# Kernel tuning notes

Hardware: AMD Instinct MI355X
Metric: run time of the kernel (lower is better)

## Reference

```python
import jax, jax.numpy as jnp
import numpy as np

B, N, F, H, ITERS = 128, 512, 8, 128, 3


def setup_inputs() -> dict:
    key = jax.random.key(0)
    ks = jax.random.split(key, 20)
    s = lambda d: 1.0 / np.sqrt(d)
    inp = {
        "jets": jax.random.normal(ks[0], (B, N, F), dtype=jnp.float32),
        "mask": jnp.ones((B, N), dtype=jnp.float32),
        # embedding: 2-layer MLP (emb_init=2)
        "emb_W0": jax.random.normal(ks[1], (F, H), jnp.float32) * s(F),
        "emb_b0": jnp.zeros((H,), jnp.float32),
        "emb_W1": jax.random.normal(ks[2], (H, H), jnp.float32) * s(H),
        "emb_b1": jnp.zeros((H,), jnp.float32),
        # MP layers (stacked over iters): message MLP + vertex update MLP
        "mp_Wm": jax.random.normal(ks[3], (ITERS, H, H), jnp.float32) * s(H),
        "mp_bm": jnp.zeros((ITERS, H), jnp.float32),
        "mp_Wu": jax.random.normal(ks[4], (ITERS, 2 * H, H), jnp.float32) * s(2 * H),
        "mp_bu": jnp.zeros((ITERS, H), jnp.float32),
        # simple readout: sum-pool then 2-layer MLP
        "ro_W1": jax.random.normal(ks[5], (H, H), jnp.float32) * s(H),
        "ro_b1": jnp.zeros((H,), jnp.float32),
        "ro_W2": jax.random.normal(ks[6], (H, H), jnp.float32) * s(H),
        "ro_b2": jnp.zeros((H,), jnp.float32),
    }
    return inp


def _adjacency(jets, mask):
    # fixed Gaussian-kernel affinity on raw features, row-softmax normalized
    sq = jnp.sum(jets * jets, axis=-1)                      # [B,N]
    d2 = sq[:, :, None] + sq[:, None, :] - 2.0 * jnp.einsum("bif,bjf->bij", jets, jets)
    logits = -d2 + jnp.where(mask[:, None, :] > 0, 0.0, -1e9)  # mask columns
    return jax.nn.softmax(logits, axis=-1)                  # [B,N,N]


def reference(jets, mask, emb_W0, emb_b0, emb_W1, emb_b1,
              mp_Wm, mp_bm, mp_Wu, mp_bu, ro_W1, ro_b1, ro_W2, ro_b2):
    # embedding
    h = jax.nn.relu(jnp.einsum("bnf,fh->bnh", jets, emb_W0) + emb_b0)
    h = jax.nn.relu(jnp.einsum("bnh,hk->bnk", h, emb_W1) + emb_b1)
    dij = _adjacency(jets, mask)                            # fixed across iterations
    m3 = mask[:, :, None]
    for t in range(ITERS):  # small fixed iteration count
        msg = jax.nn.relu(jnp.einsum("bnh,hk->bnk", h, mp_Wm[t]) + mp_bm[t])
        agg = jnp.einsum("bij,bjh->bih", dij, msg)          # gather+aggregate over adjacency
        h = jax.nn.relu(jnp.einsum("bnh,hk->bnk", jnp.concatenate([h, agg], axis=-1), mp_Wu[t]) + mp_bu[t])
        h = h * m3
    pooled = jnp.sum(h * m3, axis=1)                        # [B,H]
    out = jax.nn.relu(pooled @ ro_W1 + ro_b1) @ ro_W2 + ro_b2
    return out
```

## Files before the change

kernel.cpp:

```cpp
#include <hip/hip_runtime.h>
#include <stdint.h>
#include <stddef.h>

#define Bb 128
#define Nn 512
#define Hh 128
#define ROWS (Bb*Nn)

typedef __bf16 bf16;
typedef __bf16 bf16x2 __attribute__((ext_vector_type(2)));
typedef __bf16 bf16x4 __attribute__((ext_vector_type(4)));
typedef __bf16 bf16x8 __attribute__((ext_vector_type(8)));
typedef float  f32x4  __attribute__((ext_vector_type(4)));

__device__ __forceinline__ void glds16(const void* g, void* l) {
  __builtin_amdgcn_global_load_lds(
      (const __attribute__((address_space(1))) void*)g,
      (__attribute__((address_space(3))) void*)l, 16, 0, 0);
}


__global__ __launch_bounds__(256) void prep_pmat(
    const float* __restrict__ eW1, const float* __restrict__ Wm,
    const float* __restrict__ Wu, bf16* __restrict__ WTe,
    bf16* __restrict__ WmF, bf16* __restrict__ WuF,
    const float* __restrict__ jets, const float* __restrict__ mask,
    bf16* __restrict__ PF, float* __restrict__ rsum) {
  __shared__ float Xs[Nn*9];
  __shared__ float cbs[Nn];
  const int t = threadIdx.x;
  if (blockIdx.x >= 512) {
    int idx = (blockIdx.x - 512)*256 + t;
    if (idx < 16384) {
      int k = idx >> 7, c = idx & 127;
      WTe[c*128 + (k ^ ((c & 7) << 3))] = (bf16)eW1[idx];
    } else if (idx < 65536) {
      int sub = idx - 16384;
      int s = sub >> 14, r = sub & 16383;
      int k = r >> 7, c = r & 127;
      WmF[s*16384 + (((c>>4)*4 + (k>>5))*64 + ((k>>3)&3)*16 + (c&15))*8 + (k&7)] = (bf16)Wm[sub];
    } else {
      int sub = idx - 65536;
      int s = sub >> 15, r = sub & 32767;
      int k = r >> 7, c = r & 127;
      WuF[s*32768 + (((c>>4)*8 + (k>>5))*64 + ((k>>3)&3)*16 + (c&15))*8 + (k&7)] = (bf16)Wu[sub];
    }
    return;
  }
  const int b = blockIdx.x & 127, ic = blockIdx.x >> 7;
  const int i0 = ic*128;
  const float* jb = jets + (size_t)b*Nn*8;
  for (int j = t; j < Nn; j += 256) {
    float s2 = 0.f;
#pragma unroll
    for (int f = 0; f < 8; ++f) { float v = jb[j*8+f]; Xs[j*9+f] = v; s2 = fmaf(v,v,s2); }
    cbs[j] = s2 + (mask[(size_t)b*Nn+j] > 0.f ? 0.f : 1e9f);
  }
  __syncthreads();
  const int w = t >> 6, lane = t & 63, l15 = lane & 15, g = lane >> 4;
  const int i0w = i0 + w*32;
  float xi2[2][8], sqi[2], lsum[2];
#pragma unroll
  for (int r = 0; r < 2; ++r) {
    int i = i0w + r*16 + l15;
    float sq = 0.f;
#pragma unroll
    for (int f = 0; f < 8; ++f) {
      float v = Xs[i*9+f];
      xi2[r][f] = 2.f*v;
      sq = fmaf(v, v, sq);
    }
    sqi[r] = sq;
    lsum[r] = 0.f;
  }
  bf16* Pr[2];
#pragma unroll
  for (int r = 0; r < 2; ++r) {
    int it = (i0w >> 4) + r;
    Pr[r] = PF + (((size_t)b*32 + it)*16)*512 + lane*8;
  }
#pragma unroll 2
  for (int j0 = 0; j0 < Nn; j0 += 32) {
    bf16x8 pfr[2];
#pragma unroll
    for (int e = 0; e < 8; ++e) {
      int j = j0 + 8*g + e;
      float xj[8];
#pragma unroll
      for (int f = 0; f < 8; ++f) xj[f] = Xs[j*9+f];
      float cb = cbs[j];
      float d0 = -(cb + sqi[0]);
      float d1 = -(cb + sqi[1]);
#pragma unroll
      for (int f = 0; f < 8; ++f) {
        d0 = fmaf(xi2[0][f], xj[f], d0);
        d1 = fmaf(xi2[1][f], xj[f], d1);
      }
      float ev0 = __expf(d0), ev1 = __expf(d1);
      lsum[0] += ev0; lsum[1] += ev1;
      pfr[0][e] = (bf16)ev0;
      pfr[1][e] = (bf16)ev1;
    }
#pragma unroll
    for (int r = 0; r < 2; ++r)
      *(bf16x8*)(Pr[r] + (j0 >> 5)*512) = pfr[r];
  }
#pragma unroll
  for (int r = 0; r < 2; ++r) {
    float s = lsum[r];
    s += __shfl_xor(s, 16, 64);
    s += __shfl_xor(s, 32, 64);
    if (g == 0) rsum[(size_t)b*Nn + i0w + r*16 + l15] = 1.f/s;
  }
}

__global__ __launch_bounds__(256) void embed_msg0(
    const float* __restrict__ jets, const float* __restrict__ W0,
    const float* __restrict__ b0, const bf16* __restrict__ WTe,
    const float* __restrict__ b1, const bf16* __restrict__ WmF0,
    const float* __restrict__ bm0, bf16* __restrict__ h,
    bf16* __restrict__ msgF) {
  __shared__ float sW0[8*128];
  __shared__ float sb0[128];
  __shared__ bf16 h0s[128*128];
  __shared__ bf16 sWT[128*128];
  const int t = threadIdx.x;
  const int w = t >> 6, lane = t & 63, l15 = lane & 15, g = lane >> 4;
  const int row_blk = blockIdx.x*128;
  for (int q = w; q < 32; q += 4)
    glds16((const char*)WTe + q*1024 + lane*16, (char*)(void*)sWT + q*1024);
  for (int i = t; i < 8*128; i += 256) sW0[i] = W0[i];
  if (t < 128) sb0[t] = b0[t];
  __syncthreads();
  {
    const int row = t & 127, colbase = (t >> 7) * 64;
    const float4* jp = (const float4*)(jets + ((size_t)row_blk + row)*8);
    float4 x0 = jp[0], x1 = jp[1];
    float x[8] = {x0.x,x0.y,x0.z,x0.w,x1.x,x1.y,x1.z,x1.w};
    const int sw = (row & 7) << 3;
#pragma unroll
    for (int cg = 0; cg < 16; ++cg) {
      int c0 = colbase + cg*4;
      bf16x4 o;
#pragma unroll
      for (int j = 0; j < 4; ++j) {
        float a = sb0[c0+j];
#pragma unroll
        for (int f = 0; f < 8; ++f) a = fmaf(x[f], sW0[f*128 + c0 + j], a);
        o[j] = (bf16)fmaxf(a, 0.f);
      }
      *(bf16x4*)(h0s + row*128 + (c0 ^ sw)) = o;
    }
  }
  __syncthreads();
  const int wr = (w & 1)*64, wc = (w >> 1)*64;
  f32x4 acc[4][4];
#pragma unroll
  for (int m = 0; m < 4; ++m)
#pragma unroll
    for (int n = 0; n < 4; ++n) acc[m][n] = (f32x4){0.f,0.f,0.f,0.f};
#pragma unroll
  for (int kk = 0; kk < 128; kk += 32) {
    bf16x8 bfr[4], wfr[4];
#pragma unroll
    for (int n = 0; n < 4; ++n) {
      int row = wr + n*16 + l15;
      bfr[n] = *(const bf16x8*)(h0s + row*128 + ((kk + 8*g) ^ ((row & 7) << 3)));
    }
#pragma unroll
    for (int m = 0; m < 4; ++m) {
      int c = wc + m*16 + l15;
      wfr[m] = *(const bf16x8*)(sWT + c*128 + ((kk + 8*g) ^ ((c & 7) << 3)));
    }
#pragma unroll
    for (int m = 0; m < 4; ++m)
#pragma unroll
      for (int n = 0; n < 4; ++n)
        acc[m][n] = __builtin_amdgcn_mfma_f32_16x16x32_bf16(wfr[m], bfr[n], acc[m][n], 0,0,0);
  }
  __syncthreads();
#pragma unroll
  for (int m = 0; m < 4; ++m) {
    f32x4 bs = *(const f32x4*)(b1 + wc + m*16 + g*4);
#pragma unroll
    for (int n = 0; n < 4; ++n) {
      int lr = wr + n*16 + l15;
      int r = row_blk + lr;
      int c0 = wc + m*16 + g*4;
      bf16x4 o;
#pragma unroll
      for (int j = 0; j < 4; ++j) o[j] = (bf16)fmaxf(acc[m][n][j] + bs[j], 0.f);
      *(bf16x4*)(h + (size_t)r*128 + c0) = o;
      *(bf16x4*)(h0s + lr*128 + (c0 ^ ((lr & 7) << 3))) = o;
    }
  }
  __syncthreads();
  {
    f32x4 acc2[4][4];
#pragma unroll
    for (int m = 0; m < 4; ++m)
#pragma unroll
      for (int n = 0; n < 4; ++n) acc2[m][n] = (f32x4){0.f,0.f,0.f,0.f};
#pragma unroll
    for (int kk = 0; kk < 128; kk += 32) {
      bf16x8 bfr[4], wfr[4];
#pragma unroll
      for (int n = 0; n < 4; ++n) {
        int lr = wr + n*16 + l15;
        bfr[n] = *(const bf16x8*)(h0s + lr*128 + ((kk + 8*g) ^ ((lr & 7) << 3)));
      }
#pragma unroll
      for (int m = 0; m < 4; ++m) {
        int cblk = (wc >> 4) + m;
        wfr[m] = *(const bf16x8*)(WmF0 + (size_t)(cblk*4 + (kk >> 5))*512 + lane*8);
      }
#pragma unroll
      for (int m = 0; m < 4; ++m)
#pragma unroll
        for (int n = 0; n < 4; ++n)
          acc2[m][n] = __builtin_amdgcn_mfma_f32_16x16x32_bf16(bfr[n], wfr[m], acc2[m][n], 0,0,0);
    }
    const int b = row_blk >> 9;
    const int rbase = (row_blk & 511) + wr;
#pragma unroll
    for (int m = 0; m < 4; ++m) {
      int c = wc + m*16 + l15;
      int mblk = (wc >> 4) + m;
      float bc = bm0[c];
#pragma unroll
      for (int n = 0; n < 4; ++n) {
        int rl = rbase + n*16 + g*4;
        bf16x4 o;
#pragma unroll
        for (int j = 0; j < 4; ++j) o[j] = (bf16)fmaxf(acc2[m][n][j] + bc, 0.f);
        size_t off = (size_t)b*65536 + (size_t)((rl>>5)*8 + mblk)*512
                   + (((rl>>3)&3)*16 + l15)*8 + (rl&7);
        *(bf16x4*)(msgF + off) = o;
      }
    }
  }
}

template<bool DO_MSG>
__global__ __launch_bounds__(256, 1) void iter_fused(
    const bf16* __restrict__ PF, const float* __restrict__ rsum,
    const float* __restrict__ mask, const bf16* __restrict__ msgFin,
    bf16* __restrict__ h,
    const bf16* __restrict__ WuF, const float* __restrict__ bu,
    const bf16* __restrict__ WmF, const float* __restrict__ bm,
    bf16* __restrict__ msgFout) {
  __shared__ __align__(16) char smem[65536];
  bf16* htile = (bf16*)smem;
  bf16* aggs  = (bf16*)(smem + 32768);
  const int t = threadIdx.x;
  const int b  = blockIdx.x & 127;
  const int ic = blockIdx.x >> 7;
  const int i0 = ic*128;
  const int w = t >> 6, lane = t & 63, l15 = lane & 15, g = lane >> 4;

  {
    const int i0w = i0 + w*32;
    float r_i[2];
#pragma unroll
    for (int r = 0; r < 2; ++r) r_i[r] = rsum[(size_t)b*Nn + i0w + r*16 + l15];
    f32x4 acc[2][8];
#pragma unroll
    for (int r = 0; r < 2; ++r)
#pragma unroll
      for (int m = 0; m < 8; ++m) acc[r][m] = (f32x4){0.f,0.f,0.f,0.f};
    const bf16* mBF = msgFin + (size_t)b*65536 + lane*8;
    const bf16* pBF = PF + ((size_t)b*32 + (i0w >> 4))*16*512 + lane*8;

    bf16x8 afrA[8], afrB[8], pfrA[2], pfrB[2];
    auto loadA = [&](int kt) {
#pragma unroll
      for (int m = 0; m < 8; ++m) afrA[m] = *(const bf16x8*)(mBF + (kt*8 + m)*512);
      pfrA[0] = *(const bf16x8*)(pBF + kt*512);
      pfrA[1] = *(const bf16x8*)(pBF + (16 + kt)*512);
    };
    auto loadB = [&](int kt) {
#pragma unroll
      for (int m = 0; m < 8; ++m) afrB[m] = *(const bf16x8*)(mBF + (kt*8 + m)*512);
      pfrB[0] = *(const bf16x8*)(pBF + kt*512);
      pfrB[1] = *(const bf16x8*)(pBF + (16 + kt)*512);
    };
    auto compute = [&](const bf16x8* afr, const bf16x8* pfr) {
#pragma unroll
      for (int m = 0; m < 8; ++m) {
        acc[0][m] = __builtin_amdgcn_mfma_f32_16x16x32_bf16(afr[m], pfr[0], acc[0][m], 0,0,0);
        acc[1][m] = __builtin_amdgcn_mfma_f32_16x16x32_bf16(afr[m], pfr[1], acc[1][m], 0,0,0);
      }
    };

    loadA(0);
#pragma unroll
    for (int kt = 0; kt < 16; kt += 2) {
      loadB(kt + 1);
      compute(afrA, pfrA);
      if (kt + 2 < 16) loadA(kt + 2);
      compute(afrB, pfrB);
    }
#pragma unroll
    for (int r = 0; r < 2; ++r) {
      int lr = w*32 + r*16 + l15;
#pragma unroll
      for (int m = 0; m < 8; ++m) {
        bf16x4 o;
#pragma unroll
        for (int j = 0; j < 4; ++j) o[j] = (bf16)(acc[r][m][j] * r_i[r]);
        int c0 = m*16 + g*4;
        *(bf16x4*)(aggs + lr*128 + (c0 ^ ((lr & 7) << 3))) = o;
      }
    }
  }
  __syncthreads();

  const int wr = (w & 1)*64, wc = (w >> 1)*64;
  const size_t growbase = (size_t)b*Nn + i0;
  {
    f32x4 acc[4][4];
#pragma unroll
    for (int m = 0; m < 4; ++m)
#pragma unroll
      for (int n = 0; n < 4; ++n) acc[m][n] = (f32x4){0.f,0.f,0.f,0.f};
#pragma unroll
    for (int kk = 0; kk < 256; kk += 32) {
      bf16x8 bfr[4];
      if (kk < 128) {
#pragma unroll
        for (int n = 0; n < 4; ++n)
          bfr[n] = *(const bf16x8*)(h + (growbase + wr + n*16 + l15)*128 + kk + 8*g);
      } else {
#pragma unroll
        for (int n = 0; n < 4; ++n) {
          int lr = wr + n*16 + l15;
          int kl = (kk - 128) + 8*g;
          bfr[n] = *(const bf16x8*)(aggs + lr*128 + (kl ^ ((lr & 7) << 3)));
        }
      }
      bf16x8 wfr[4];
#pragma unroll
      for (int m = 0; m < 4; ++m) {
        int cblk = (wc >> 4) + m;
        wfr[m] = *(const bf16x8*)(WuF + (size_t)(cblk*8 + (kk >> 5))*512 + lane*8);
      }
#pragma unroll
      for (int m = 0; m < 4; ++m)
#pragma unroll
        for (int n = 0; n < 4; ++n)
          acc[m][n] = __builtin_amdgcn_mfma_f32_16x16x32_bf16(wfr[m], bfr[n], acc[m][n], 0,0,0);
    }
    __syncthreads();
#pragma unroll
    for (int m = 0; m < 4; ++m) {
      f32x4 bs = *(const f32x4*)(bu + wc + m*16 + g*4);
#pragma unroll
      for (int n = 0; n < 4; ++n) {
        int lr = wr + n*16 + l15;
        size_t r = growbase + lr;
        float mv = mask[r];
        bf16x4 o;
#pragma unroll
        for (int j = 0; j < 4; ++j)
          o[j] = (bf16)(fmaxf(acc[m][n][j] + bs[j], 0.f) * mv);
        int c0 = wc + m*16 + g*4;
        *(bf16x4*)(h + r*128 + c0) = o;
        if (DO_MSG)
          *(bf16x4*)(htile + lr*128 + (c0 ^ ((lr & 7) << 3))) = o;
      }
    }
  }
  if (!DO_MSG) return;
  __syncthreads();

  {
    f32x4 acc[4][4];
#pragma unroll
    for (int m = 0; m < 4; ++m)
#pragma unroll
      for (int n = 0; n < 4; ++n) acc[m][n] = (f32x4){0.f,0.f,0.f,0.f};
#pragma unroll
    for (int kk = 0; kk < 128; kk += 32) {
      bf16x8 bfr[4], wfr[4];
#pragma unroll
      for (int n = 0; n < 4; ++n) {
        int lr = wr + n*16 + l15;
        bfr[n] = *(const bf16x8*)(htile + lr*128 + ((kk + 8*g) ^ ((lr & 7) << 3)));
      }
#pragma unroll
      for (int m = 0; m < 4; ++m) {
        int cblk = (wc >> 4) + m;
        wfr[m] = *(const bf16x8*)(WmF + (size_t)(cblk*4 + (kk >> 5))*512 + lane*8);
      }
#pragma unroll
      for (int m = 0; m < 4; ++m)
#pragma unroll
        for (int n = 0; n < 4; ++n)
          acc[m][n] = __builtin_amdgcn_mfma_f32_16x16x32_bf16(bfr[n], wfr[m], acc[m][n], 0,0,0);
    }
#pragma unroll
    for (int m = 0; m < 4; ++m) {
      int c = wc + m*16 + l15;
      int mblk = (wc >> 4) + m;
      float bc = bm[c];
#pragma unroll
      for (int n = 0; n < 4; ++n) {
        int rl = i0 + wr + n*16 + g*4;
        bf16x4 o;
#pragma unroll
        for (int j = 0; j < 4; ++j) o[j] = (bf16)fmaxf(acc[m][n][j] + bc, 0.f);
        size_t off = (size_t)b*65536 + (size_t)((rl>>5)*8 + mblk)*512
                   + (((rl>>3)&3)*16 + l15)*8 + (rl&7);
        *(bf16x4*)(msgFout + off) = o;
      }
    }
  }
}

__global__ __launch_bounds__(256) void pool_readout(
    const bf16* __restrict__ h, const float* __restrict__ mask,
    const float* __restrict__ W1, const float* __restrict__ b1,
    const float* __restrict__ W2, const float* __restrict__ b2,
    float* __restrict__ out) {
  __shared__ float part[3][128];
  __shared__ float pl[128];
  __shared__ float hid[128];
  int b = blockIdx.x, t = threadIdx.x, g = t >> 6, cp = (t & 63)*2;
  float a0 = 0.f, a1 = 0.f;
  for (int n = g*128; n < g*128+128; ++n) {
    float mv = mask[(size_t)b*Nn + n];
    bf16x2 v = *(const bf16x2*)(h + ((size_t)b*Nn + n)*128 + cp);
    a0 = fmaf((float)v[0], mv, a0);
    a1 = fmaf((float)v[1], mv, a1);
  }
  if (g > 0) { part[g-1][cp] = a0; part[g-1][cp+1] = a1; }
  __syncthreads();
  if (g == 0) {
    pl[cp]   = a0 + part[0][cp]   + part[1][cp]   + part[2][cp];
    pl[cp+1] = a1 + part[0][cp+1] + part[1][cp+1] + part[2][cp+1];
  }
  __syncthreads();
  if (t < 128) {
    float a = b1[t];
#pragma unroll 4
    for (int j = 0; j < 128; ++j) a = fmaf(pl[j], W1[j*128 + t], a);
    hid[t] = fmaxf(a, 0.f);
  }
  __syncthreads();
  if (t < 128) {
    float a = b2[t];
#pragma unroll 4
    for (int j = 0; j < 128; ++j) a = fmaf(hid[j], W2[j*128 + t], a);
    out[(size_t)b*128 + t] = a;
  }
}

extern "C" void kernel_launch(void* const* d_in, const int* in_sizes, int n_in,
                              void* d_out, int out_size, void* d_ws, size_t ws_size,
                              hipStream_t stream) {
  const float* jets = (const float*)d_in[0];
  const float* mask = (const float*)d_in[1];
  const float* eW0  = (const float*)d_in[2];
  const float* eb0  = (const float*)d_in[3];
  const float* eW1  = (const float*)d_in[4];
  const float* eb1  = (const float*)d_in[5];
  const float* Wm   = (const float*)d_in[6];
  const float* bm   = (const float*)d_in[7];
  const float* Wu   = (const float*)d_in[8];
  const float* bu   = (const float*)d_in[9];
  const float* rW1  = (const float*)d_in[10];
  const float* rb1  = (const float*)d_in[11];
  const float* rW2  = (const float*)d_in[12];
  const float* rb2  = (const float*)d_in[13];
  float* out = (float*)d_out;

  bf16* h     = (bf16*)d_ws;
  bf16* msgFA = h     + (size_t)ROWS*128;
  bf16* msgFB = msgFA + (size_t)ROWS*128;
  bf16* PF    = msgFB + (size_t)ROWS*128;
  bf16* WTe   = PF    + (size_t)Bb*512*512;
  bf16* WmF   = WTe   + 128*128;
  bf16* WuF   = WmF   + 3*128*128;
  float* rsum = (float*)(WuF + 3*256*128);

  prep_pmat<<<512 + 640, 256, 0, stream>>>(eW1, Wm, Wu, WTe, WmF, WuF,
                                           jets, mask, PF, rsum);
  embed_msg0<<<ROWS/128, 256, 0, stream>>>(jets, eW0, eb0, WTe, eb1,
                                           WmF, bm, h, msgFA);
  iter_fused<true><<<Bb*4, 256, 0, stream>>>(
      PF, rsum, mask, msgFA, h,
      WuF, bu, WmF + (size_t)1*128*128, bm + 1*128, msgFB);
  iter_fused<true><<<Bb*4, 256, 0, stream>>>(
      PF, rsum, mask, msgFB, h,
      WuF + (size_t)1*256*128, bu + 1*128,
      WmF + (size_t)2*128*128, bm + 2*128, msgFA);
  iter_fused<false><<<Bb*4, 256, 0, stream>>>(
      PF, rsum, mask, msgFA, h,
      WuF + (size_t)2*256*128, bu + 2*128, nullptr, nullptr, nullptr);

  pool_readout<<<Bb, 256, 0, stream>>>(h, mask, rW1, rb1, rW2, rb2, out);
}
```

Baseline: 159.1 us.

## Stage shared message tiles into LDS via async global_load_lds double buffering

The aggregation GEMM previously had every wave read the same message fragments directly from global memory into registers. Those fragments are now staged cooperatively into a double-buffered 64KB LDS region with global_load_lds, four k-steps at a time, and each wave reads its MFMA operands from LDS. This removes the four-fold redundant global reads across waves and overlaps the next stage's loads with the current compute. In exchange it adds block-wide barriers, LDS traffic, and reuse of the htile/aggs LDS space as the staging buffer.

```diff
diff --git a/kernel.cpp b/kernel.cpp
--- a/kernel.cpp
+++ b/kernel.cpp
@@ -268,38 +268,48 @@
     for (int r = 0; r < 2; ++r)
 #pragma unroll
       for (int m = 0; m < 8; ++m) acc[r][m] = (f32x4){0.f,0.f,0.f,0.f};
-    const bf16* mBF = msgFin + (size_t)b*65536 + lane*8;
-    const bf16* pBF = PF + ((size_t)b*32 + (i0w >> 4))*16*512 + lane*8;
-
-    bf16x8 afrA[8], afrB[8], pfrA[2], pfrB[2];
-    auto loadA = [&](int kt) {
-#pragma unroll
-      for (int m = 0; m < 8; ++m) afrA[m] = *(const bf16x8*)(mBF + (kt*8 + m)*512);
-      pfrA[0] = *(const bf16x8*)(pBF + kt*512);
-      pfrA[1] = *(const bf16x8*)(pBF + (16 + kt)*512);
+    const char* mSrc = (const char*)(msgFin + (size_t)b*65536);
+    const bf16* pBF  = PF + ((size_t)b*32 + (i0w >> 4))*16*512 + lane*8;
+
+    auto stage = [&](int ktBase, int half) {
+      const char* src = mSrc + ktBase*8192;
+      char* dst = (char*)smem + half*32768;
+      for (int q = w; q < 32; q += 4)
+        glds16(src + q*1024 + lane*16, dst + q*1024);
     };
-    auto loadB = [&](int kt) {
-#pragma unroll
-      for (int m = 0; m < 8; ++m) afrB[m] = *(const bf16x8*)(mBF + (kt*8 + m)*512);
-      pfrB[0] = *(const bf16x8*)(pBF + kt*512);
-      pfrB[1] = *(const bf16x8*)(pBF + (16 + kt)*512);
+    auto computeQ = [&](int ktBase, int half) {
+      const bf16* sbase = (const bf16*)((const char*)smem + half*32768);
+      bf16x8 pq[8];
+#pragma unroll
+      for (int k2 = 0; k2 < 4; ++k2) {
+        pq[k2*2]   = *(const bf16x8*)(pBF + (ktBase + k2)*512);
+        pq[k2*2+1] = *(const bf16x8*)(pBF + (16 + ktBase + k2)*512);
+      }
+#pragma unroll
+      for (int k2 = 0; k2 < 4; ++k2) {
+        bf16x8 afr[8];
+#pragma unroll
+        for (int m = 0; m < 8; ++m)
+          afr[m] = *(const bf16x8*)(sbase + (k2*8 + m)*512 + lane*8);
+#pragma unroll
+        for (int m = 0; m < 8; ++m) {
+          acc[0][m] = __builtin_amdgcn_mfma_f32_16x16x32_bf16(afr[m], pq[k2*2],   acc[0][m], 0,0,0);
+          acc[1][m] = __builtin_amdgcn_mfma_f32_16x16x32_bf16(afr[m], pq[k2*2+1], acc[1][m], 0,0,0);
+        }
+      }
     };
-    auto compute = [&](const bf16x8* afr, const bf16x8* pfr) {
-#pragma unroll
-      for (int m = 0; m < 8; ++m) {
-        acc[0][m] = __builtin_amdgcn_mfma_f32_16x16x32_bf16(afr[m], pfr[0], acc[0][m], 0,0,0);
-        acc[1][m] = __builtin_amdgcn_mfma_f32_16x16x32_bf16(afr[m], pfr[1], acc[1][m], 0,0,0);
-      }
-    };
-
-    loadA(0);
-#pragma unroll
-    for (int kt = 0; kt < 16; kt += 2) {
-      loadB(kt + 1);
-      compute(afrA, pfrA);
-      if (kt + 2 < 16) loadA(kt + 2);
-      compute(afrB, pfrB);
-    }
+
+    stage(0, 0);
+    __syncthreads();
+    stage(4, 1);  computeQ(0, 0);
+    __syncthreads();
+    stage(8, 0);  computeQ(4, 1);
+    __syncthreads();
+    stage(12, 1); computeQ(8, 0);
+    __syncthreads();
+    computeQ(12, 1);
+    __syncthreads();
+
 #pragma unroll
     for (int r = 0; r < 2; ++r) {
       int lr = w*32 + r*16 + l15;
```

Measured after the change: 158.7 us. Within noise of the previous version (-0.3%).
